# Kernel optimization log

Hardware: AMD Instinct MI355X
Metric: run time of the kernel (lower is better)

The kernel has to match this reference:

```python
import jax, jax.numpy as jnp
import numpy as np

DIM = 512
NUM_HEADS = 8
HEAD_DIM = DIM // NUM_HEADS


def setup_inputs() -> dict:
    key = jax.random.key(0)
    ks = jax.random.split(key, 9)
    s = 1.0 / np.sqrt(DIM)
    x = jax.random.normal(ks[0], (2, 4096, DIM), dtype=jnp.float32)
    Wq = jax.random.uniform(ks[1], (DIM, DIM), jnp.float32, -s, s)
    bq = jax.random.uniform(ks[2], (DIM,), jnp.float32, -s, s)
    Wk = jax.random.uniform(ks[3], (DIM, DIM), jnp.float32, -s, s)
    bk = jax.random.uniform(ks[4], (DIM,), jnp.float32, -s, s)
    Wv = jax.random.uniform(ks[5], (DIM, DIM), jnp.float32, -s, s)
    bv = jax.random.uniform(ks[6], (DIM,), jnp.float32, -s, s)
    Wo = jax.random.uniform(ks[7], (DIM, DIM), jnp.float32, -s, s)
    bo = jax.random.uniform(ks[8], (DIM,), jnp.float32, -s, s)
    return {"x": x, "Wq": Wq, "bq": bq, "Wk": Wk, "bk": bk,
            "Wv": Wv, "bv": bv, "Wo": Wo, "bo": bo}


def reference(x, Wq, bq, Wk, bk, Wv, bv, Wo, bo):
    B, S, D = x.shape
    H, Hd = NUM_HEADS, HEAD_DIM
    # Linear layers (torch stores weight as [out,in]; here W is [in,out])
    q = (x @ Wq + bq).reshape(B, S, H, Hd).transpose(0, 2, 1, 3)  # [B,H,S,Hd]
    k = (x @ Wk + bk).reshape(B, S, H, Hd).transpose(0, 2, 1, 3)
    v = (x @ Wv + bv).reshape(B, S, H, Hd).transpose(0, 2, 1, 3)
    # NOTE: original scales by dim**0.5, not head_dim**0.5
    energy = jnp.einsum('bhqd,bhkd->bhqk', q, k) / jnp.sqrt(jnp.float32(D))
    attn = jax.nn.softmax(energy, axis=-1)
    out = jnp.einsum('bhqk,bhkd->bhqd', attn, v)
    out = out.transpose(0, 2, 1, 3).reshape(B, S, D)
    return out @ Wo + bo
```

## Files before the change

kernel.cpp:

```cpp
#include <hip/hip_runtime.h>

typedef unsigned short USH;
typedef short s16x8 __attribute__((ext_vector_type(8)));
typedef float f32x4 __attribute__((ext_vector_type(4)));
typedef float f32x4v __attribute__((ext_vector_type(4)));
typedef unsigned int u32x4 __attribute__((ext_vector_type(4)));
typedef s16x8 s16x8_a __attribute__((may_alias));
typedef f32x4v f32x4v_a __attribute__((may_alias));
typedef u32x4 u32x4_a __attribute__((may_alias));
typedef unsigned long long u64_a __attribute__((may_alias));

#if __has_builtin(__builtin_amdgcn_exp2f)
#define EXP2F(x) __builtin_amdgcn_exp2f(x)
#else
#define EXP2F(x) __builtin_exp2f(x)
#endif

__device__ __forceinline__ USH f2bf(float f) {
  union { float f; unsigned int i; } c; c.f = f;
  unsigned int x = c.i;
  return (USH)((x + 0x7FFFu + ((x >> 16) & 1u)) >> 16);
}
__device__ __forceinline__ unsigned int pk_bf16(float a, float b) {
#if __has_builtin(__builtin_amdgcn_cvt_pk_bf16_f32)
  typedef USH ush2 __attribute__((ext_vector_type(2)));
  union { ush2 v; unsigned int u; } r;
  r.v = __builtin_amdgcn_cvt_pk_bf16_f32(a, b);
  return r.u;
#else
  union { float f; unsigned int i; } ca, cb; ca.f = a; cb.f = b;
  return ((ca.i + 0x8000u) >> 16) | ((cb.i + 0x8000u) & 0xFFFF0000u);
#endif
}

__device__ __forceinline__ f32x4 mfma16(s16x8 a, s16x8 b, f32x4 c) {
  return __builtin_amdgcn_mfma_f32_16x16x32_bf16(a, b, c, 0, 0, 0);
}

#if __has_builtin(__builtin_amdgcn_global_load_lds)
__device__ __forceinline__ void gld_lds16(const USH* g, USH* l) {
  __builtin_amdgcn_global_load_lds(
      static_cast<const unsigned int __attribute__((address_space(1)))*>(
          (const void __attribute__((address_space(1)))*)g),
      static_cast<unsigned int __attribute__((address_space(3)))*>(
          (void __attribute__((address_space(3)))*)l),
      16, 0, 0);
}
#else
__device__ __forceinline__ void gld_lds16(const USH* g, USH* l) {
  *(s16x8_a*)l = *(const s16x8_a*)g;
}
#endif

__global__ __launch_bounds__(256) void prep(
    const float* __restrict__ Wq, const float* __restrict__ Wk,
    const float* __restrict__ Wv, const float* __restrict__ Wo,
    const float* __restrict__ x, USH* __restrict__ wsT, USH* __restrict__ xb) {
  __shared__ float tile[32][33];
  const int z = blockIdx.z;
  const int t = threadIdx.x;
  if (z == 4) {
    const size_t b0 = ((size_t)blockIdx.y * 16 + blockIdx.x) * 16384;
    #pragma unroll
    for (int j = 0; j < 8; ++j) {
      const size_t i = b0 + (size_t)j * 2048 + t * 8;
      const f32x4v a = *(const f32x4v_a*)(x + i);
      const f32x4v b = *(const f32x4v_a*)(x + i + 4);
      u32x4 s;
      s.x = pk_bf16(a.x, a.y); s.y = pk_bf16(a.z, a.w);
      s.z = pk_bf16(b.x, b.y); s.w = pk_bf16(b.z, b.w);
      *(u32x4_a*)(xb + i) = s;
    }
    return;
  }
  const float* W = (z == 0) ? Wq : (z == 1) ? Wk : (z == 2) ? Wv : Wo;
  USH* WT = wsT + (size_t)z * 262144;
  const int n0 = blockIdx.x * 32, k0 = blockIdx.y * 32;
  const int tx = t & 31, ty = t >> 5;
  #pragma unroll
  for (int i = 0; i < 4; ++i)
    tile[ty + i * 8][tx] = W[(size_t)(k0 + ty + i * 8) * 512 + n0 + tx];
  __syncthreads();
  #pragma unroll
  for (int i = 0; i < 4; ++i)
    WT[(size_t)(n0 + ty + i * 8) * 512 + k0 + tx] = f2bf(tile[tx][ty + i * 8]);
}

template <int MODE>
__global__ __launch_bounds__(256, 3) void gemm_bias(
    const USH* __restrict__ A, const USH* __restrict__ BT0,
    const float* __restrict__ b0, const float* __restrict__ b1,
    const float* __restrict__ b2,
    USH* __restrict__ oQ, USH* __restrict__ oKV, float* __restrict__ oF) {
  __shared__ __align__(16) USH As[128 * 68];
  __shared__ __align__(16) USH Bs[128 * 68];
  const int z = blockIdx.z;
  const USH* BT = BT0 + (size_t)z * 262144;
  const float* bias = (z == 0) ? b0 : ((z == 1) ? b1 : b2);
  USH* outb = (z == 0) ? oQ : (oKV + (size_t)(z - 1) * 4194304);
  const float qs = (MODE == 1 && z == 0) ? 0.06375871528132839f : 1.0f;

  const int t = threadIdx.x;
  const int w = t >> 6, lane = t & 63;
  const int c = lane & 15, g = lane >> 4;
  const int wm = w & 1, wn = w >> 1;
  const int m0 = blockIdx.x * 128, n0 = blockIdx.y * 128;
  const int srow = t >> 1, scol = (t & 1) * 32;

  f32x4 acc[4][4] = {};

  const USH* Ap0 = A + (size_t)(m0 + srow) * 512 + scol;
  const USH* Bp0 = BT + (size_t)(n0 + srow) * 512 + scol;
  s16x8 pa[4], pb[4];
  #pragma unroll
  for (int j = 0; j < 4; ++j) {
    pa[j] = *(const s16x8_a*)(Ap0 + j * 8);
    pb[j] = *(const s16x8_a*)(Bp0 + j * 8);
  }

  for (int kt = 0; kt < 8; ++kt) {
    __syncthreads();
    #pragma unroll
    for (int j = 0; j < 4; ++j) {
      *(s16x8_a*)(As + srow * 68 + scol + j * 8) = pa[j];
      *(s16x8_a*)(Bs + srow * 68 + scol + j * 8) = pb[j];
    }
    const int ktn = (kt < 7) ? kt + 1 : kt;
    #pragma unroll
    for (int j = 0; j < 4; ++j) {
      pa[j] = *(const s16x8_a*)(Ap0 + ktn * 64 + j * 8);
      pb[j] = *(const s16x8_a*)(Bp0 + ktn * 64 + j * 8);
    }
    __syncthreads();
    #pragma unroll
    for (int ks = 0; ks < 2; ++ks) {
      s16x8 af[4], bfr[4];
      #pragma unroll
      for (int i = 0; i < 4; ++i) {
        af[i]  = *(const s16x8_a*)(As + (wm * 64 + i * 16 + c) * 68 + ks * 32 + g * 8);
        bfr[i] = *(const s16x8_a*)(Bs + (wn * 64 + i * 16 + c) * 68 + ks * 32 + g * 8);
      }
      #pragma unroll
      for (int mf = 0; mf < 4; ++mf)
        #pragma unroll
        for (int nf = 0; nf < 4; ++nf)
          acc[mf][nf] = mfma16(af[mf], bfr[nf], acc[mf][nf]);
    }
  }

  #pragma unroll
  for (int nf = 0; nf < 4; ++nf) {
    const int n = n0 + wn * 64 + nf * 16 + c;
    const float bv = bias[n];
    #pragma unroll
    for (int mf = 0; mf < 4; ++mf)
      #pragma unroll
      for (int r = 0; r < 4; ++r) {
        const int m = m0 + wm * 64 + mf * 16 + g * 4 + r;
        const float v = (acc[mf][nf][r] + bv) * qs;
        if (MODE == 0) {
          oF[(size_t)m * 512 + n] = v;
        } else {
          const int bb = m >> 12, s = m & 4095, h = n >> 6, hd = n & 63;
          if (z == 2)
            outb[(((size_t)(bb * 8 + h)) * 64 + hd) * 4096 + s] = f2bf(v);
          else
            outb[(((size_t)(bb * 8 + h)) * 4096 + s) * 64 + hd] = f2bf(v);
        }
      }
  }
}

__global__ __launch_bounds__(512, 4) void attn(const USH* __restrict__ Qbuf,
                                               const USH* __restrict__ kv,
                                               USH* __restrict__ att) {
  __shared__ __align__(16) USH Ks[2 * 4096];
  __shared__ __align__(16) USH Vt[2 * 4096];
  __shared__ __align__(16) USH Ps[8][16 * 76];
  __shared__ float lbuf[8][16];

  const int t = threadIdx.x;
  const int w = t >> 6, lane = t & 63;
  const int c = lane & 15, g = lane >> 4;
  const int bh = blockIdx.y;
  const int bb = bh >> 3, hh = bh & 7;
  const size_t base = (size_t)bh * 262144;
  const USH* Q = Qbuf + base;
  const USH* K = kv + base;
  const USH* V = kv + 4194304 + base;
  const int q0 = blockIdx.x * 128 + w * 16;

  s16x8 qf[2];
  #pragma unroll
  for (int kh = 0; kh < 2; ++kh)
    qf[kh] = *(const s16x8_a*)(Q + (size_t)(q0 + c) * 64 + kh * 32 + g * 8);

  s16x8 onesf;
  {
    const short one = (short)0x3F80, val = (c == 0) ? one : (short)0;
    #pragma unroll
    for (int j = 0; j < 8; ++j) onesf[j] = val;
  }

  f32x4 o[4] = {};
  f32x4 o_l = {};

  const int pK = w * 16 + (lane >> 2);
  const int keyK = pK & 63, halfK = pK >> 6;
  const int ccK = (lane & 3) ^ ((keyK >> 1) & 3);
  const USH* gK0 = K + (size_t)keyK * 64 + halfK * 32 + ccK * 8;
  const int hdV = w * 8 + (lane >> 3);
  const int ccV = (lane & 7) ^ (hdV & 7);
  const USH* gV0 = V + (size_t)hdV * 4096 + ccV * 8;
  USH* lK = Ks + w * 512 + lane * 8;
  USH* lV = Vt + w * 512 + lane * 8;

  gld_lds16(gK0, lK);
  gld_lds16(gV0, lV);

  for (int kt = 0; kt < 64; ++kt) {
    const int buf = kt & 1;
    __syncthreads();
    if (kt < 63) {
      const int nb = (buf ^ 1) * 4096;
      gld_lds16(gK0 + (size_t)(kt + 1) * 4096, lK + nb);
      gld_lds16(gV0 + (size_t)(kt + 1) * 64, lV + nb);
    }

    f32x4 st[4] = {};
    #pragma unroll
    for (int kh = 0; kh < 2; ++kh) {
      s16x8 ak[4];
      #pragma unroll
      for (int kff = 0; kff < 4; ++kff) {
        const int row = kff * 16 + c;
        const int qsw = (g ^ ((c >> 1) & 3)) * 8;
        ak[kff] = *(const s16x8_a*)(Ks + buf * 4096 + kh * 2048 + row * 32 + qsw);
      }
      #pragma unroll
      for (int kff = 0; kff < 4; ++kff)
        st[kff] = mfma16(ak[kff], qf[kh], st[kff]);
    }

    #pragma unroll
    for (int kff = 0; kff < 4; ++kff)
      #pragma unroll
      for (int r = 0; r < 4; ++r)
        st[kff][r] = EXP2F(st[kff][r]);

    #pragma unroll
    for (int kff = 0; kff < 4; ++kff) {
      const unsigned int lo = pk_bf16(st[kff][0], st[kff][1]);
      const unsigned int hi = pk_bf16(st[kff][2], st[kff][3]);
      *(u64_a*)(&Ps[w][c * 76 + kff * 16 + g * 4]) =
          (unsigned long long)lo | ((unsigned long long)hi << 32);
    }

    #pragma unroll
    for (int kf = 0; kf < 2; ++kf) {
      const s16x8 ap = *(const s16x8_a*)(&Ps[w][c * 76 + kf * 32 + g * 8]);
      s16x8 bv[4];
      #pragma unroll
      for (int hf = 0; hf < 4; ++hf) {
        const int qv = ((kf * 4 + g) ^ (c & 7)) * 8;
        bv[hf] = *(const s16x8_a*)(Vt + buf * 4096 + (c + 16 * hf) * 64 + qv);
      }
      #pragma unroll
      for (int hf = 0; hf < 4; ++hf)
        o[hf] = mfma16(ap, bv[hf], o[hf]);
      o_l = mfma16(ap, onesf, o_l);
    }
  }

  if (c == 0) {
    #pragma unroll
    for (int r = 0; r < 4; ++r) lbuf[w][g * 4 + r] = o_l[r];
  }
  __syncthreads();

  #pragma unroll
  for (int r = 0; r < 4; ++r) {
    const int ml = g * 4 + r;
    const float linv = 1.0f / lbuf[w][ml];
    const int qrow = q0 + ml;
    #pragma unroll
    for (int hf = 0; hf < 4; ++hf) {
      const int hd = c + 16 * hf;
      att[((size_t)(bb * 4096 + qrow)) * 512 + hh * 64 + hd] =
          f2bf(o[hf][r] * linv);
    }
  }
}

extern "C" void kernel_launch(void* const* d_in, const int* in_sizes, int n_in,
                              void* d_out, int out_size, void* d_ws, size_t ws_size,
                              hipStream_t stream) {
  (void)in_sizes; (void)n_in; (void)out_size; (void)ws_size;
  const float* x  = (const float*)d_in[0];
  const float* Wq = (const float*)d_in[1];
  const float* bq = (const float*)d_in[2];
  const float* Wk = (const float*)d_in[3];
  const float* bk = (const float*)d_in[4];
  const float* Wv = (const float*)d_in[5];
  const float* bv = (const float*)d_in[6];
  const float* Wo = (const float*)d_in[7];
  const float* bo = (const float*)d_in[8];
  USH* ws  = (USH*)d_ws;
  USH* wT  = ws;
  USH* kv  = ws + 1048576;
  USH* att = ws + 1048576 + 8388608;
  float* outF = (float*)d_out;
  USH* qscratch = (USH*)d_out;
  USH* xb = (USH*)d_out + 4194304;

  prep<<<dim3(16, 16, 5), 256, 0, stream>>>(Wq, Wk, Wv, Wo, x, wT, xb);
  gemm_bias<1><<<dim3(64, 4, 3), 256, 0, stream>>>(xb, wT, bq, bk, bv,
                                                   qscratch, kv, nullptr);
  attn<<<dim3(32, 16), 512, 0, stream>>>(qscratch, kv, att);
  gemm_bias<0><<<dim3(64, 4, 1), 256, 0, stream>>>(att, wT + 3 * 262144, bo, bo, bo,
                                                   nullptr, nullptr, outF);
}
```

Before: 208.3 us.

## Process two query fragments per wave in attention to reuse K/V LDS loads

Each wave of the attention kernel now handles 32 query rows (two 16-row fragments) instead of 16. The K and V fragments read from LDS are reused across both, which halves LDS traffic and global K/V tile loads per query. In exchange the grid shrinks to 256 blocks, which may underfill the GPU's compute units, and launch bounds drop to 2 blocks per CU to allow more registers.

Result: no change. 212.3 us (+1.9%).

```diff
diff --git a/kernel.cpp b/kernel.cpp
--- a/kernel.cpp
+++ b/kernel.cpp
@@ -171,13 +171,13 @@
   }
 }
 
-__global__ __launch_bounds__(512, 4) void attn(const USH* __restrict__ Qbuf,
+__global__ __launch_bounds__(512, 2) void attn(const USH* __restrict__ Qbuf,
                                                const USH* __restrict__ kv,
                                                USH* __restrict__ att) {
   __shared__ __align__(16) USH Ks[2 * 4096];
   __shared__ __align__(16) USH Vt[2 * 4096];
   __shared__ __align__(16) USH Ps[8][16 * 76];
-  __shared__ float lbuf[8][16];
+  __shared__ float lbuf[8][32];
 
   const int t = threadIdx.x;
   const int w = t >> 6, lane = t & 63;
@@ -188,12 +188,14 @@
   const USH* Q = Qbuf + base;
   const USH* K = kv + base;
   const USH* V = kv + 4194304 + base;
-  const int q0 = blockIdx.x * 128 + w * 16;
-
-  s16x8 qf[2];
-  #pragma unroll
-  for (int kh = 0; kh < 2; ++kh)
-    qf[kh] = *(const s16x8_a*)(Q + (size_t)(q0 + c) * 64 + kh * 32 + g * 8);
+  const int q0 = blockIdx.x * 256 + w * 32;
+
+  s16x8 qf[2][2];
+  #pragma unroll
+  for (int colf = 0; colf < 2; ++colf)
+    #pragma unroll
+    for (int kh = 0; kh < 2; ++kh)
+      qf[colf][kh] = *(const s16x8_a*)(Q + (size_t)(q0 + colf * 16 + c) * 64 + kh * 32 + g * 8);
 
   s16x8 onesf;
   {
@@ -202,8 +204,8 @@
     for (int j = 0; j < 8; ++j) onesf[j] = val;
   }
 
-  f32x4 o[4] = {};
-  f32x4 o_l = {};
+  f32x4 o[2][4] = {};
+  f32x4 o_l[2] = {};
 
   const int pK = w * 16 + (lane >> 2);
   const int keyK = pK & 63, halfK = pK >> 6;
@@ -227,69 +229,81 @@
       gld_lds16(gV0 + (size_t)(kt + 1) * 64, lV + nb);
     }
 
-    f32x4 st[4] = {};
-    #pragma unroll
-    for (int kh = 0; kh < 2; ++kh) {
-      s16x8 ak[4];
+    s16x8 ak[2][4];
+    #pragma unroll
+    for (int kh = 0; kh < 2; ++kh)
       #pragma unroll
       for (int kff = 0; kff < 4; ++kff) {
         const int row = kff * 16 + c;
         const int qsw = (g ^ ((c >> 1) & 3)) * 8;
-        ak[kff] = *(const s16x8_a*)(Ks + buf * 4096 + kh * 2048 + row * 32 + qsw);
-      }
-      #pragma unroll
-      for (int kff = 0; kff < 4; ++kff)
-        st[kff] = mfma16(ak[kff], qf[kh], st[kff]);
-    }
-
-    #pragma unroll
-    for (int kff = 0; kff < 4; ++kff)
-      #pragma unroll
-      for (int r = 0; r < 4; ++r)
-        st[kff][r] = EXP2F(st[kff][r]);
-
-    #pragma unroll
-    for (int kff = 0; kff < 4; ++kff) {
-      const unsigned int lo = pk_bf16(st[kff][0], st[kff][1]);
-      const unsigned int hi = pk_bf16(st[kff][2], st[kff][3]);
-      *(u64_a*)(&Ps[w][c * 76 + kff * 16 + g * 4]) =
-          (unsigned long long)lo | ((unsigned long long)hi << 32);
-    }
-
-    #pragma unroll
-    for (int kf = 0; kf < 2; ++kf) {
-      const s16x8 ap = *(const s16x8_a*)(&Ps[w][c * 76 + kf * 32 + g * 8]);
-      s16x8 bv[4];
+        ak[kh][kff] = *(const s16x8_a*)(Ks + buf * 4096 + kh * 2048 + row * 32 + qsw);
+      }
+    s16x8 bv[2][4];
+    #pragma unroll
+    for (int kf = 0; kf < 2; ++kf)
       #pragma unroll
       for (int hf = 0; hf < 4; ++hf) {
         const int qv = ((kf * 4 + g) ^ (c & 7)) * 8;
-        bv[hf] = *(const s16x8_a*)(Vt + buf * 4096 + (c + 16 * hf) * 64 + qv);
-      }
-      #pragma unroll
-      for (int hf = 0; hf < 4; ++hf)
-        o[hf] = mfma16(ap, bv[hf], o[hf]);
-      o_l = mfma16(ap, onesf, o_l);
+        bv[kf][hf] = *(const s16x8_a*)(Vt + buf * 4096 + (c + 16 * hf) * 64 + qv);
+      }
+
+    #pragma unroll
+    for (int colf = 0; colf < 2; ++colf) {
+      f32x4 st[4] = {};
+      #pragma unroll
+      for (int kh = 0; kh < 2; ++kh)
+        #pragma unroll
+        for (int kff = 0; kff < 4; ++kff)
+          st[kff] = mfma16(ak[kh][kff], qf[colf][kh], st[kff]);
+
+      #pragma unroll
+      for (int kff = 0; kff < 4; ++kff)
+        #pragma unroll
+        for (int r = 0; r < 4; ++r)
+          st[kff][r] = EXP2F(st[kff][r]);
+
+      #pragma unroll
+      for (int kff = 0; kff < 4; ++kff) {
+        const unsigned int lo = pk_bf16(st[kff][0], st[kff][1]);
+        const unsigned int hi = pk_bf16(st[kff][2], st[kff][3]);
+        *(u64_a*)(&Ps[w][c * 76 + kff * 16 + g * 4]) =
+            (unsigned long long)lo | ((unsigned long long)hi << 32);
+      }
+
+      #pragma unroll
+      for (int kf = 0; kf < 2; ++kf) {
+        const s16x8 ap = *(const s16x8_a*)(&Ps[w][c * 76 + kf * 32 + g * 8]);
+        #pragma unroll
+        for (int hf = 0; hf < 4; ++hf)
+          o[colf][hf] = mfma16(ap, bv[kf][hf], o[colf][hf]);
+        o_l[colf] = mfma16(ap, onesf, o_l[colf]);
+      }
     }
   }
 
   if (c == 0) {
     #pragma unroll
-    for (int r = 0; r < 4; ++r) lbuf[w][g * 4 + r] = o_l[r];
+    for (int colf = 0; colf < 2; ++colf)
+      #pragma unroll
+      for (int r = 0; r < 4; ++r)
+        lbuf[w][colf * 16 + g * 4 + r] = o_l[colf][r];
   }
   __syncthreads();
 
   #pragma unroll
-  for (int r = 0; r < 4; ++r) {
-    const int ml = g * 4 + r;
-    const float linv = 1.0f / lbuf[w][ml];
-    const int qrow = q0 + ml;
-    #pragma unroll
-    for (int hf = 0; hf < 4; ++hf) {
-      const int hd = c + 16 * hf;
-      att[((size_t)(bb * 4096 + qrow)) * 512 + hh * 64 + hd] =
-          f2bf(o[hf][r] * linv);
-    }
-  }
+  for (int colf = 0; colf < 2; ++colf)
+    #pragma unroll
+    for (int r = 0; r < 4; ++r) {
+      const int ml = colf * 16 + g * 4 + r;
+      const float linv = 1.0f / lbuf[w][ml];
+      const int qrow = q0 + ml;
+      #pragma unroll
+      for (int hf = 0; hf < 4; ++hf) {
+        const int hd = c + 16 * hf;
+        att[((size_t)(bb * 4096 + qrow)) * 512 + hh * 64 + hd] =
+            f2bf(o[colf][hf][r] * linv);
+      }
+    }
 }
 
 extern "C" void kernel_launch(void* const* d_in, const int* in_sizes, int n_in,
@@ -316,7 +330,7 @@
   prep<<<dim3(16, 16, 5), 256, 0, stream>>>(Wq, Wk, Wv, Wo, x, wT, xb);
   gemm_bias<1><<<dim3(64, 4, 3), 256, 0, stream>>>(xb, wT, bq, bk, bv,
                                                    qscratch, kv, nullptr);
-  attn<<<dim3(32, 16), 512, 0, stream>>>(qscratch, kv, att);
+  attn<<<dim3(16, 16), 512, 0, stream>>>(qscratch, kv, att);
   gemm_bias<0><<<dim3(64, 4, 1), 256, 0, stream>>>(att, wT + 3 * 262144, bo, bo, bo,
                                                    nullptr, nullptr, outF);
 }
```
